# Kernel optimization log

Measured on AMD Instinct MI355X. Metric: run time of the kernel, lower is better.

## Reference

```python
import jax, jax.numpy as jnp
import numpy as np

# Constants derived from init_kwargs / input shapes
B = 4          # number of graphs (equal-sized point clouds)
N = 16384      # points per graph
STRIDE = 4     # center_sampler: strided sampling, ratio 0.25 -> M = N/4
K = 20         # k nearest neighbors
N_SCAL = 16    # reps '16x0+16x1': 16 scalars
N_VEC = 16     # 16 vectors (3 coeffs each)
D = N_SCAL + 3 * N_VEC   # 64 feature coeffs
HID = 128
OUT = 128


def transform_coeffs(x, R):
    """TensorReps('16x0+16x1') coefficient transform: scalars unchanged,
    each 3-vector v -> R @ v.  x: [n, D], R: [n, 3, 3]."""
    s = x[:, :N_SCAL]
    v = x[:, N_SCAL:].reshape(-1, N_VEC, 3)
    v = jnp.einsum('nab,nkb->nka', R, v)
    return jnp.concatenate([s, v.reshape(-1, 3 * N_VEC)], axis=-1)


def setup_inputs() -> dict:
    key = jax.random.key(0)
    ks = jax.random.split(key, 6)
    Ntot = B * N
    x = jax.random.normal(ks[0], (Ntot, D), jnp.float32)
    pos = jax.random.normal(ks[1], (Ntot, 3), jnp.float32)
    # orthonormal local frames via QR of random 3x3 matrices
    lf = jax.random.normal(ks[2], (Ntot, 3, 3), jnp.float32)
    lframes, _ = jnp.linalg.qr(lf)
    batch = jnp.repeat(jnp.arange(B, dtype=jnp.int32), N)
    W1 = jax.random.normal(ks[3], (2 * D, HID), jnp.float32) / np.sqrt(2 * D)
    b1 = jnp.zeros((HID,), jnp.float32)
    W2 = jax.random.normal(ks[4], (HID, OUT), jnp.float32) / np.sqrt(HID)
    b2 = jnp.zeros((OUT,), jnp.float32)
    return {"x": x, "pos": pos, "lframes": lframes, "batch": batch,
            "W1": W1, "b1": b1, "W2": W2, "b2": b2}


def reference(x, pos, lframes, batch, W1, b1, W2, b2):
    M = N // STRIDE
    # --- center_sampler: strided sampling per graph (CustomPointSampler) ---
    idx = (jnp.arange(B)[:, None] * N + jnp.arange(0, N, STRIDE)[None, :]).reshape(-1)  # [B*M]

    # --- transform features to global frame: coeffs with lframes^T ---
    kf = transform_coeffs(x, jnp.swapaxes(lframes, -1, -2))
    # --- concat_pos_to_features (transform_pos=False) ---
    kf = jnp.concatenate([kf, pos], axis=-1)            # [Ntot, 67]
    Dk = kf.shape[-1]

    # --- brute-force per-graph kNN: centers query against all nodes ---
    kf_b = kf.reshape(B, N, Dk)
    q = kf_b[:, ::STRIDE]                               # [B, M, Dk] centers
    d2 = (jnp.sum(q * q, -1)[:, :, None]
          + jnp.sum(kf_b * kf_b, -1)[:, None, :]
          - 2.0 * jnp.einsum('bmd,bnd->bmn', q, kf_b))  # [B, M, N]
    _, nbr = jax.lax.top_k(-d2, K)                      # [B, M, K] per-graph idx
    src = nbr + (jnp.arange(B) * N)[:, None, None]      # global node idx

    # --- gather dst/src node data ---
    x_dst = x[idx].reshape(B, M, D)
    lf_dst = lframes[idx]                               # [B*M, 3, 3]
    x_src = x[src.reshape(-1)].reshape(B, M, K, D)

    # --- EdgeConv (tensor-frames flavor): relative features rotated into the
    #     destination local frame, MLP over [x_i, R_i (x_j - x_i)], max-aggr ---
    rel = x_src - x_dst[:, :, None]                     # [B, M, K, D]
    R_edge = jnp.repeat(lf_dst, K, axis=0)              # [B*M*K, 3, 3]
    rel_local = transform_coeffs(rel.reshape(-1, D), R_edge).reshape(B, M, K, D)
    h = jnp.concatenate(
        [jnp.broadcast_to(x_dst[:, :, None], rel.shape), rel_local], axis=-1)  # [B,M,K,2D]
    msg = jax.nn.relu(h @ W1 + b1) @ W2 + b2            # [B, M, K, OUT]
    out = jnp.max(msg, axis=2).reshape(B * M, OUT)

    return out, pos[idx], batch[idx], lf_dst
```

## Files before the change

### kernel.cpp

```cpp
#include <hip/hip_runtime.h>
#include <hip/hip_bf16.h>

#define NTOT 65536
#define KNN  20
#define KROW 104

typedef __attribute__((ext_vector_type(4))) float f32x4;
typedef __attribute__((ext_vector_type(8))) short s16x8;

#define WS_NORM 13631488
#define WS_WT1  15204352
#define WS_WT2  15237120
#define WS_MG   15269888

#define ROWS 144
#define CSTR 257
#define OFF_TAUG 149056
#define KNN_SMEM 149312
#define THRESH 64

__device__ __forceinline__ unsigned short f2bf_rne(float v){
  unsigned u = __float_as_uint(v);
  return (unsigned short)((u + 0x7FFFu + ((u >> 16) & 1u)) >> 16);
}

__global__ __launch_bounds__(256) void k_prep(const float* __restrict__ x,
        const float* __restrict__ pos, const float* __restrict__ lfr,
        unsigned short* __restrict__ kfB, float* __restrict__ normB){
  int n = blockIdx.x * 256 + threadIdx.x;
  const float* xr = x + n * 64;
  float R[9];
  #pragma unroll
  for (int j = 0; j < 9; j++) R[j] = lfr[n * 9 + j];
  float c[67];
  #pragma unroll
  for (int i = 0; i < 16; i++) c[i] = xr[i];
  #pragma unroll
  for (int k = 0; k < 16; k++){
    float v0 = xr[16 + 3*k], v1 = xr[17 + 3*k], v2 = xr[18 + 3*k];
    #pragma unroll
    for (int a = 0; a < 3; a++)
      c[16 + 3*k + a] = R[a] * v0 + R[3 + a] * v1 + R[6 + a] * v2;
  }
  #pragma unroll
  for (int a = 0; a < 3; a++) c[64 + a] = pos[n * 3 + a];
  float sq = 0.f;
  #pragma unroll
  for (int d = 0; d < 67; d++) sq += c[d] * c[d];
  __attribute__((aligned(16))) unsigned short row[KROW];
  #pragma unroll
  for (int d = 0; d < 67; d++) row[d] = f2bf_rne(c[d]);
  #pragma unroll
  for (int d = 67; d < KROW; d++) row[d] = 0;
  uint4* dst = (uint4*)(kfB + (size_t)n * KROW);
  const uint4* s4 = (const uint4*)row;
  #pragma unroll
  for (int i = 0; i < 13; i++) dst[i] = s4[i];
  normB[n] = sq;
}

__global__ __launch_bounds__(256) void k_wprep(const float* __restrict__ W1,
        const float* __restrict__ W2, unsigned short* __restrict__ wb1,
        unsigned short* __restrict__ wb2){
  int a = blockIdx.x * 256 + threadIdx.x;
  int kb = a >> 12, n = (a >> 5) & 127, kl = a & 31;
  int i = ((kb << 5) + kl) * 128 + n;
  wb1[a] = f2bf_rne(W1[i]);
  wb2[a] = f2bf_rne(W2[i]);
}

__device__ __forceinline__ unsigned col_compact32(unsigned* buf,
    int col, int cn, int lane){
  unsigned e0 = (lane < cn) ? buf[lane * CSTR + col] : 0xFFFFFFFFu;
  unsigned e1 = (lane + 64 < cn) ? buf[(lane + 64) * CSTR + col] : 0xFFFFFFFFu;
  unsigned T = 0;
  #pragma unroll 1
  for (int b = 31; b >= 0; --b){
    unsigned cand = T | (1u << b);
    int c = __popcll(__ballot(e0 < cand)) + __popcll(__ballot(e1 < cand));
    if (c <= 31) T = cand;
  }
  unsigned long long m0 = __ballot(e0 <= T);
  unsigned long long m1 = __ballot(e1 <= T);
  int b1 = __popcll(m0);
  unsigned long long ltm = (1ull << lane) - 1ull;
  if (e0 <= T) buf[__popcll(m0 & ltm) * CSTR + col] = e0;
  if (e1 <= T) buf[(b1 + __popcll(m1 & ltm)) * CSTR + col] = e1;
  return T;
}

__device__ __forceinline__ unsigned col_compact18(unsigned* buf,
    int col, int cn, int lane){
  unsigned e0 = (lane < cn) ? buf[lane * CSTR + col] : 0xFFFFFFFFu;
  unsigned e1 = (lane + 64 < cn) ? buf[(lane + 64) * CSTR + col] : 0xFFFFFFFFu;
  unsigned T = 0;
  #pragma unroll 1
  for (int b = 31; b >= 14; --b){
    unsigned cand = T | (1u << b);
    int c = __popcll(__ballot(e0 < cand)) + __popcll(__ballot(e1 < cand));
    if (c <= 31) T = cand;
  }
  unsigned th = T >> 14;
  unsigned long long m0 = __ballot((e0 >> 14) <= th);
  unsigned long long m1 = __ballot((e1 >> 14) <= th);
  int b1 = __popcll(m0);
  int kc = b1 + __popcll(m1);
  unsigned long long ltm = (1ull << lane) - 1ull;
  if ((e0 >> 14) <= th) buf[__popcll(m0 & ltm) * CSTR + col] = e0;
  if ((e1 >> 14) <= th) buf[(b1 + __popcll(m1 & ltm)) * CSTR + col] = e1;
  return T | (unsigned)kc;
}

__global__ __launch_bounds__(1024, 4) void k_knn(
    const unsigned short* __restrict__ kfB, const float* __restrict__ normB,
    unsigned short* __restrict__ mgG){
  __shared__ __attribute__((aligned(16))) char smem[KNN_SMEM];
  unsigned* buf = (unsigned*)smem;
  unsigned* tauG = (unsigned*)(smem + OFF_TAUG);

  int tid = threadIdx.x;
  int blk = blockIdx.x;
  int b = blk & 3;
  int qloc0 = (blk >> 2) << 6;
  int bbase = b << 14;

  if (tid < 64) tauG[tid] = 0x7F7FC000u;

  int lane = tid & 63;
  int wv = tid >> 6;
  int wq = wv >> 2;
  int kq = wv & 3;
  int l15 = lane & 15, quad = lane >> 4;
  int colB = (wq << 6) + kq;

  int qloc = qloc0 + (wq << 4);
  s16x8 af[3];
  {
    int nodeA = bbase + ((qloc + l15) << 2);
    const unsigned short* ap = kfB + (size_t)nodeA * KROW + quad * 8;
    af[0] = *(const s16x8*)(ap);
    af[1] = *(const s16x8*)(ap + 32);
    af[2] = *(const s16x8*)(ap + 64);
  }
  float qsq[4];
  #pragma unroll
  for (int r = 0; r < 4; r++)
    qsq[r] = normB[bbase + ((qloc + (quad << 2) + r) << 2)];

  float tauR[4] = {3.0e38f, 3.0e38f, 3.0e38f, 3.0e38f};
  int cntR[4];

  const unsigned short* kp = kfB + (size_t)(bbase + (kq << 12) + l15) * KROW + quad * 8;
  const float* np = normB + (bbase + (kq << 12) + l15);

  __syncthreads();

  s16x8 cK[4][3];
  float nK[4];
  #define LOADK(S) do { \
      cK[S][0] = *(const s16x8*)(kp); \
      cK[S][1] = *(const s16x8*)(kp + 32); \
      cK[S][2] = *(const s16x8*)(kp + 64); \
      nK[S] = *np; kp += 16 * KROW; np += 16; } while (0)

  auto comp = [&](const s16x8 bf[3], float ksqv, float d2v[4]){
    f32x4 acc = (f32x4){0.f, 0.f, 0.f, 0.f};
    acc = __builtin_amdgcn_mfma_f32_16x16x32_bf16(af[0], bf[0], acc, 0, 0, 0);
    acc = __builtin_amdgcn_mfma_f32_16x16x32_bf16(af[1], bf[1], acc, 0, 0, 0);
    acc = __builtin_amdgcn_mfma_f32_16x16x32_bf16(af[2], bf[2], acc, 0, 0, 0);
    #pragma unroll
    for (int r = 0; r < 4; r++)
      d2v[r] = fmaxf(qsq[r] + ksqv - 2.f * acc[r], 0.f);
  };

  auto seed = [&](const float d2v[4], int g){
    int kidx = (kq << 12) + (g << 4) + l15;
    #pragma unroll
    for (int r = 0; r < 4; r++){
      unsigned pk = ((__float_as_uint(d2v[r]) + 0x2000u) & 0xFFFFC000u) | (unsigned)kidx;
      buf[((g << 4) + l15) * CSTR + colB + (quad << 4) + (r << 2)] = pk;
    }
  };

  auto process = [&](const float d2v[4], int g){
    bool p[4];
    #pragma unroll
    for (int r = 0; r < 4; r++) p[r] = d2v[r] < tauR[r];
    if (__any(p[0] | p[1] | p[2] | p[3])){
      int kidx = (kq << 12) + (g << 4) + l15;
      #pragma unroll
      for (int r = 0; r < 4; r++){
        unsigned long long m = __ballot(p[r]);
        if (m){
          int lo = (int)((m >> (quad << 4)) & 0xFFFFull);
          if (lo){
            int colr = colB + (quad << 4) + (r << 2);
            int pre = __popc(lo & ((1 << l15) - 1));
            if (p[r]){
              unsigned pk = ((__float_as_uint(d2v[r]) + 0x2000u) & 0xFFFFC000u) | (unsigned)kidx;
              buf[(cntR[r] + pre) * CSTR + colr] = pk;
            }
            cntR[r] += __popc(lo);
          }
        }
      }
    }
  };

  auto check_compact = [&](int limit){
    #pragma unroll
    for (int r = 0; r < 4; r++){
      unsigned long long mr = __ballot(cntR[r] > limit);
      while (mr){
        int ldr = __ffsll((unsigned long long)mr) - 1;
        int qd = ldr >> 4;
        mr &= ~(0xFFFFull << (qd << 4));
        int col = colB + (qd << 4) + (r << 2);
        int cn = __shfl(cntR[r], qd << 4, 64);
        unsigned Tk = col_compact18(buf, col, cn, lane);
        if (quad == qd) cntR[r] = (int)(Tk & 0x3FFFu);
        if (lane == 0) atomicMin(&tauG[(wq << 4) + (qd << 2) + r], Tk & 0xFFFFC000u);
      }
    }
  };

  float d2v[4];
  LOADK(0); LOADK(1); LOADK(2); LOADK(3);
  #pragma unroll
  for (int j = 0; j < 4; j++){
    comp(cK[j], nK[j], d2v);
    seed(d2v, j);
    LOADK(j);
  }
  #pragma unroll
  for (int r = 0; r < 4; r++) cntR[r] = 64;

  #pragma unroll 1
  for (int g = 4; g < 256; g += 4){
    #pragma unroll
    for (int j = 0; j < 4; j++){
      comp(cK[j], nK[j], d2v);
      LOADK(j);
      process(d2v, g + j);
    }
    check_compact(THRESH);
    uint4 tg = *(const uint4*)&tauG[(wq << 4) + (quad << 2)];
    tauR[0] = __uint_as_float(tg.x & 0xFFFFC000u);
    tauR[1] = __uint_as_float(tg.y & 0xFFFFC000u);
    tauR[2] = __uint_as_float(tg.z & 0xFFFFC000u);
    tauR[3] = __uint_as_float(tg.w & 0xFFFFC000u);
  }

  {
    #pragma unroll
    for (int r = 0; r < 4; r++){
      unsigned long long mr = __ballot(cntR[r] > 32);
      while (mr){
        int ldr = __ffsll((unsigned long long)mr) - 1;
        int qd = ldr >> 4;
        mr &= ~(0xFFFFull << (qd << 4));
        int col = colB + (qd << 4) + (r << 2);
        int cn = __shfl(cntR[r], qd << 4, 64);
        col_compact32(buf, col, cn, lane);
        if (quad == qd) cntR[r] = 32;
      }
    }
  }
  __syncthreads();

  #pragma unroll 1
  for (int s = 0; s < 4; s++){
    int q = (wv << 2) + s;
    int qid = (b << 12) + qloc0 + q;
    unsigned e0 = buf[(lane & 31) * CSTR + (q << 2) + (lane >> 5)];
    unsigned e1 = buf[(lane & 31) * CSTR + (q << 2) + 2 + (lane >> 5)];
    unsigned T = 0;
    #pragma unroll 1
    for (int bb = 31; bb >= 0; --bb){
      unsigned cand = T | (1u << bb);
      int c = __popcll(__ballot(e0 < cand)) + __popcll(__ballot(e1 < cand));
      if (c <= 31) T = cand;
    }
    unsigned long long m0 = __ballot(e0 <= T);
    unsigned long long m1 = __ballot(e1 <= T);
    int b1 = __popcll(m0);
    unsigned long long ltm = (1ull << lane) - 1ull;
    int p0 = __popcll(m0 & ltm);
    int p1 = b1 + __popcll(m1 & ltm);
    if ((e0 <= T) && (p0 < 32)) mgG[qid * 32 + p0] = (unsigned short)(e0 & 0x3FFFu);
    if ((e1 <= T) && (p1 < 32)) mgG[qid * 32 + p1] = (unsigned short)(e1 & 0x3FFFu);
  }
}

#define M_X   0
#define M_H   43520
#define M_B1  84480
#define M_B2  84992
#define M_NBR 85504
#define M_XD  86144
#define M_LF  88192
#define M_SZ  88512

__global__ __launch_bounds__(512) void k_mlp(const float* __restrict__ x,
    const float* __restrict__ pos, const float* __restrict__ lfr,
    const unsigned short* __restrict__ mgG,
    const unsigned short* __restrict__ wb1, const unsigned short* __restrict__ wb2,
    const float* __restrict__ b1, const float* __restrict__ b2,
    float* __restrict__ out){
  __shared__ __attribute__((aligned(16))) char smem[M_SZ];
  double* qkf = (double*)(smem + M_X);
  float* xsF = (float*)(smem + M_X);
  unsigned short* a1B = (unsigned short*)(smem + M_X);
  unsigned short* hB = (unsigned short*)(smem + M_H);
  float* b1L = (float*)(smem + M_B1);
  float* b2L = (float*)(smem + M_B2);
  int*   nbrL = (int*)(smem + M_NBR);
  float* xdL  = (float*)(smem + M_XD);
  float* lfL  = (float*)(smem + M_LF);

  int tid = threadIdx.x;
  int qid0 = blockIdx.x * 8;
  int lane = tid & 63, wv = tid >> 6;
  int l15 = lane & 15, quad = lane >> 4;

  s16x8 wf1[4], wf2[4];
  #pragma unroll
  for (int ks = 0; ks < 4; ks++){
    int a = (ks * 128 + (wv << 4) + l15) * 32 + (quad << 3);
    wf1[ks] = *(const s16x8*)(wb1 + a);
    wf2[ks] = *(const s16x8*)(wb2 + a);
  }

  {
    int q = tid >> 6, d = tid & 63;
    int qid = qid0 + q;
    int node = ((qid >> 12) << 14) + ((qid & 4095) << 2);
    xdL[q * 64 + d] = x[node * 64 + d];
  }
  if (tid < 72){
    int q = tid / 9, j = tid - 9 * q;
    int qid = qid0 + q;
    int node = ((qid >> 12) << 14) + ((qid & 4095) << 2);
    lfL[q * 9 + j] = lfr[node * 9 + j];
  }
  if (tid < 128){ b1L[tid] = b1[tid]; b2L[tid] = b2[tid]; }
  if (tid < 256){
    int ql = tid >> 5, j = tid & 31;
    int qid = qid0 + ql;
    int node_q = ((qid >> 12) << 14) + ((qid & 4095) << 2);
    const float* xr = x + node_q * 64;
    for (int dd = j; dd < 67; dd += 32){
      double val;
      if (dd < 16) val = (double)xr[dd];
      else if (dd < 64){
        int r = dd - 16; int k = r / 3; int a = r - 3 * k;
        val = (double)lfr[node_q*9 + a]     * (double)xr[16 + 3*k]
            + (double)lfr[node_q*9 + 3 + a] * (double)xr[17 + 3*k]
            + (double)lfr[node_q*9 + 6 + a] * (double)xr[18 + 3*k];
      } else val = (double)pos[node_q*3 + (dd - 64)];
      qkf[ql * 68 + dd] = val;
    }
  }
  __syncthreads();

  if (tid < 256){
    int ql = tid >> 5, j = tid & 31;
    int qid = qid0 + ql;
    int bbase = (qid >> 12) << 14;
    int idx = (int)mgG[(size_t)qid * 32 + j];
    int node = bbase + idx;
    const float* xr = x + node * 64;
    double R[9];
    #pragma unroll
    for (int t = 0; t < 9; t++) R[t] = (double)lfr[node * 9 + t];
    double d2 = 0.0;
    #pragma unroll
    for (int dd = 0; dd < 16; dd++){ double t = (double)xr[dd] - qkf[ql*68 + dd]; d2 += t * t; }
    #pragma unroll
    for (int k = 0; k < 16; k++){
      double v0 = xr[16 + 3*k], v1 = xr[17 + 3*k], v2 = xr[18 + 3*k];
      #pragma unroll
      for (int a = 0; a < 3; a++){
        double val = R[a] * v0 + R[3 + a] * v1 + R[6 + a] * v2;
        double t = val - qkf[ql*68 + 16 + 3*k + a]; d2 += t * t;
      }
    }
    #pragma unroll
    for (int a = 0; a < 3; a++){ double t = (double)pos[node*3 + a] - qkf[ql*68 + 64 + a]; d2 += t * t; }

    int base = (tid & 32) ? 32 : 0;
    int rank = 0;
    #pragma unroll 1
    for (int j2 = 0; j2 < 32; j2++){
      double o = __shfl(d2, base + j2, 64);
      rank += (o < d2) || ((o == d2) && (j2 < j));
    }
    if (rank < KNN) nbrL[ql * KNN + rank] = node;
  }
  __syncthreads();

  {
    int f4 = tid & 15;
    #pragma unroll
    for (int p = 0; p < 5; p++){
      int e = (tid >> 4) + (p << 5);
      float4 v = *(const float4*)&x[(size_t)nbrL[e] * 64 + (f4 << 2)];
      *(float4*)&xsF[e * 68 + (f4 << 2)] = v;
    }
  }
  __syncthreads();

  {
    int d = tid & 127, eo = tid >> 7;
    int cls, kk = 0, aa = 0;
    if (d < 64) cls = 0;
    else { int dd = d - 64;
      if (dd < 16) cls = 1;
      else { cls = 2; int r = dd - 16; kk = (r * 21846) >> 16; aa = r - 3 * kk; } }
    int hoff = ((d >> 5) * 160) * 32 + (d & 31);
    #pragma unroll 4
    for (int p = 0; p < 40; p++){
      int e = eo + (p << 2);
      int q = (e * 3277) >> 16;
      float v;
      if (cls == 0) v = xdL[q * 64 + d];
      else if (cls == 1) v = xsF[e * 68 + (d - 64)] - xdL[q * 64 + (d - 64)];
      else {
        int base = 16 + 3 * kk;
        float u0 = xsF[e * 68 + base]     - xdL[q * 64 + base];
        float u1 = xsF[e * 68 + base + 1] - xdL[q * 64 + base + 1];
        float u2 = xsF[e * 68 + base + 2] - xdL[q * 64 + base + 2];
        v = lfL[q * 9 + aa * 3] * u0 + lfL[q * 9 + aa * 3 + 1] * u1 + lfL[q * 9 + aa * 3 + 2] * u2;
      }
      hB[hoff + e * 32] = f2bf_rne(v);
    }
  }
  __syncthreads();

  {
    float b1v = b1L[(wv << 4) + l15];
    int colhi = wv >> 1, collo = ((wv & 1) << 4) + l15;
    #pragma unroll
    for (int mt = 0; mt < 10; mt++){
      f32x4 acc = (f32x4){0.f, 0.f, 0.f, 0.f};
      #pragma unroll
      for (int ks = 0; ks < 4; ks++){
        s16x8 af = *(const s16x8*)(hB + ((ks * 160 + (mt << 4) + l15) * 32 + (quad << 3)));
        acc = __builtin_amdgcn_mfma_f32_16x16x32_bf16(af, wf1[ks], acc, 0, 0, 0);
      }
      #pragma unroll
      for (int r = 0; r < 4; r++){
        float v = fmaxf(acc[r] + b1v, 0.f);
        int row = (mt << 4) + (quad << 2) + r;
        a1B[(colhi * 160 + row) * 32 + collo] = f2bf_rne(v);
      }
    }
  }
  __syncthreads();

  {
    float mxv[8];
    #pragma unroll
    for (int q = 0; q < 8; q++) mxv[q] = -3.0e38f;
    const int QA[10]  = {0,0,1,2,3,4,4,5,6,7};
    const int CUT[10] = {16,4,8,12,16,16,4,8,12,16};
    #pragma unroll
    for (int mt = 0; mt < 10; mt++){
      f32x4 acc = (f32x4){0.f, 0.f, 0.f, 0.f};
      #pragma unroll
      for (int ks = 0; ks < 4; ks++){
        s16x8 af = *(const s16x8*)(a1B + ((ks * 160 + (mt << 4) + l15) * 32 + (quad << 3)));
        acc = __builtin_amdgcn_mfma_f32_16x16x32_bf16(af, wf2[ks], acc, 0, 0, 0);
      }
      int qa = QA[mt], cut = CUT[mt];
      if (cut >= 16){
        #pragma unroll
        for (int r = 0; r < 4; r++) mxv[qa] = fmaxf(mxv[qa], acc[r]);
      } else {
        #pragma unroll
        for (int r = 0; r < 4; r++){
          int lr = (quad << 2) + r;
          bool toA = lr < cut;
          mxv[qa]     = fmaxf(mxv[qa],     toA ? acc[r] : -3.0e38f);
          mxv[qa + 1] = fmaxf(mxv[qa + 1], toA ? -3.0e38f : acc[r]);
        }
      }
    }
    #pragma unroll
    for (int q = 0; q < 8; q++){
      float v = mxv[q];
      v = fmaxf(v, __shfl_xor(v, 16, 64));
      v = fmaxf(v, __shfl_xor(v, 32, 64));
      mxv[q] = v;
    }
    if (quad == 0){
      int col = (wv << 4) + l15;
      float b2v = b2L[col];
      #pragma unroll
      for (int q = 0; q < 8; q++)
        out[(size_t)(qid0 + q) * 128 + col] = mxv[q] + b2v;
    }
  }
}

__global__ __launch_bounds__(256) void k_tail(const float* __restrict__ pos,
    const float* __restrict__ lfr, float* __restrict__ out){
  int q = blockIdx.x * 256 + threadIdx.x;
  int b = q >> 12;
  int node = (b << 14) + ((q & 4095) << 2);
  float* o_pos = out + 2097152;
  float* o_bat = out + 2146304;
  float* o_lf  = out + 2162688;
  #pragma unroll
  for (int j = 0; j < 3; j++) o_pos[q * 3 + j] = pos[node * 3 + j];
  o_bat[q] = (float)b;
  #pragma unroll
  for (int j = 0; j < 9; j++) o_lf[q * 9 + j] = lfr[node * 9 + j];
}

extern "C" void kernel_launch(void* const* d_in, const int* in_sizes, int n_in,
                              void* d_out, int out_size, void* d_ws, size_t ws_size,
                              hipStream_t stream){
  const float* x   = (const float*)d_in[0];
  const float* pos = (const float*)d_in[1];
  const float* lfr = (const float*)d_in[2];
  const float* W1  = (const float*)d_in[4];
  const float* b1  = (const float*)d_in[5];
  const float* W2  = (const float*)d_in[6];
  const float* b2  = (const float*)d_in[7];

  unsigned short* kfB = (unsigned short*)d_ws;
  float* normB = (float*)((char*)d_ws + WS_NORM);
  unsigned short* wb1 = (unsigned short*)((char*)d_ws + WS_WT1);
  unsigned short* wb2 = (unsigned short*)((char*)d_ws + WS_WT2);
  unsigned short* mgG = (unsigned short*)((char*)d_ws + WS_MG);
  float* out = (float*)d_out;

  hipLaunchKernelGGL(k_prep,   dim3(256),  dim3(256),  0, stream, x, pos, lfr, kfB, normB);
  hipLaunchKernelGGL(k_wprep,  dim3(64),   dim3(256),  0, stream, W1, W2, wb1, wb2);
  hipLaunchKernelGGL(k_knn,    dim3(256),  dim3(1024), 0, stream, kfB, normB, mgG);
  hipLaunchKernelGGL(k_mlp,    dim3(2048), dim3(512),  0, stream, x, pos, lfr, mgG, wb1, wb2, b1, b2, out);
  hipLaunchKernelGGL(k_tail,   dim3(64),   dim3(256),  0, stream, pos, lfr, out);
}
```

Before: 535.9 us.

## Shrink k_mlp blocks to 4 queries with 256 threads and 32-column warp tiles

Each k_mlp block now handles 4 query centers with 4 waves instead of 8 queries with 8 waves, which halves the LDS footprint to about 44KB. Each wave now covers 32 output columns, using two 16-column MFMA tiles that share the same A fragments, so A-fragment LDS reads are reused across the two column tiles. The goal is more resident blocks per CU and less LDS traffic. The cost is more weight fragments held in registers, twice as many blocks each reloading weights, and fewer active threads during the per-query distance and rank stage.

```diff
diff --git a/kernel.cpp b/kernel.cpp
--- a/kernel.cpp
+++ b/kernel.cpp
@@ -293,15 +293,15 @@
 }
 
 #define M_X   0
-#define M_H   43520
-#define M_B1  84480
-#define M_B2  84992
-#define M_NBR 85504
-#define M_XD  86144
-#define M_LF  88192
-#define M_SZ  88512
-
-__global__ __launch_bounds__(512) void k_mlp(const float* __restrict__ x,
+#define M_H   21760
+#define M_B1  42240
+#define M_B2  42752
+#define M_NBR 43264
+#define M_XD  43584
+#define M_LF  44608
+#define M_SZ  44752
+
+__global__ __launch_bounds__(256) void k_mlp(const float* __restrict__ x,
     const float* __restrict__ pos, const float* __restrict__ lfr,
     const unsigned short* __restrict__ mgG,
     const unsigned short* __restrict__ wb1, const unsigned short* __restrict__ wb2,
@@ -319,17 +319,19 @@
   float* lfL  = (float*)(smem + M_LF);
 
   int tid = threadIdx.x;
-  int qid0 = blockIdx.x * 8;
+  int qid0 = blockIdx.x * 4;
   int lane = tid & 63, wv = tid >> 6;
   int l15 = lane & 15, quad = lane >> 4;
 
-  s16x8 wf1[4], wf2[4];
-  #pragma unroll
-  for (int ks = 0; ks < 4; ks++){
-    int a = (ks * 128 + (wv << 4) + l15) * 32 + (quad << 3);
-    wf1[ks] = *(const s16x8*)(wb1 + a);
-    wf2[ks] = *(const s16x8*)(wb2 + a);
-  }
+  s16x8 wf1[2][4], wf2[2][4];
+  #pragma unroll
+  for (int ct = 0; ct < 2; ct++)
+    #pragma unroll
+    for (int ks = 0; ks < 4; ks++){
+      int a = (ks * 128 + (wv << 5) + (ct << 4) + l15) * 32 + (quad << 3);
+      wf1[ct][ks] = *(const s16x8*)(wb1 + a);
+      wf2[ct][ks] = *(const s16x8*)(wb2 + a);
+    }
 
   {
     int q = tid >> 6, d = tid & 63;
@@ -337,14 +339,14 @@
     int node = ((qid >> 12) << 14) + ((qid & 4095) << 2);
     xdL[q * 64 + d] = x[node * 64 + d];
   }
-  if (tid < 72){
+  if (tid < 36){
     int q = tid / 9, j = tid - 9 * q;
     int qid = qid0 + q;
     int node = ((qid >> 12) << 14) + ((qid & 4095) << 2);
     lfL[q * 9 + j] = lfr[node * 9 + j];
   }
   if (tid < 128){ b1L[tid] = b1[tid]; b2L[tid] = b2[tid]; }
-  if (tid < 256){
+  if (tid < 128){
     int ql = tid >> 5, j = tid & 31;
     int qid = qid0 + ql;
     int node_q = ((qid >> 12) << 14) + ((qid & 4095) << 2);
@@ -363,7 +365,7 @@
   }
   __syncthreads();
 
-  if (tid < 256){
+  if (tid < 128){
     int ql = tid >> 5, j = tid & 31;
     int qid = qid0 + ql;
     int bbase = (qid >> 12) << 14;
@@ -403,7 +405,7 @@
     int f4 = tid & 15;
     #pragma unroll
     for (int p = 0; p < 5; p++){
-      int e = (tid >> 4) + (p << 5);
+      int e = (tid >> 4) + (p << 4);
       float4 v = *(const float4*)&x[(size_t)nbrL[e] * 64 + (f4 << 2)];
       *(float4*)&xsF[e * 68 + (f4 << 2)] = v;
     }
@@ -417,10 +419,10 @@
     else { int dd = d - 64;
       if (dd < 16) cls = 1;
       else { cls = 2; int r = dd - 16; kk = (r * 21846) >> 16; aa = r - 3 * kk; } }
-    int hoff = ((d >> 5) * 160) * 32 + (d & 31);
+    int hoff = ((d >> 5) * 80) * 32 + (d & 31);
     #pragma unroll 4
     for (int p = 0; p < 40; p++){
-      int e = eo + (p << 2);
+      int e = eo + (p << 1);
       int q = (e * 3277) >> 16;
       float v;
       if (cls == 0) v = xdL[q * 64 + d];
@@ -438,67 +440,86 @@
   __syncthreads();
 
   {
-    float b1v = b1L[(wv << 4) + l15];
-    int colhi = wv >> 1, collo = ((wv & 1) << 4) + l15;
-    #pragma unroll
-    for (int mt = 0; mt < 10; mt++){
-      f32x4 acc = (f32x4){0.f, 0.f, 0.f, 0.f};
-      #pragma unroll
-      for (int ks = 0; ks < 4; ks++){
-        s16x8 af = *(const s16x8*)(hB + ((ks * 160 + (mt << 4) + l15) * 32 + (quad << 3)));
-        acc = __builtin_amdgcn_mfma_f32_16x16x32_bf16(af, wf1[ks], acc, 0, 0, 0);
-      }
-      #pragma unroll
-      for (int r = 0; r < 4; r++){
-        float v = fmaxf(acc[r] + b1v, 0.f);
-        int row = (mt << 4) + (quad << 2) + r;
-        a1B[(colhi * 160 + row) * 32 + collo] = f2bf_rne(v);
-      }
-    }
-  }
-  __syncthreads();
-
-  {
-    float mxv[8];
-    #pragma unroll
-    for (int q = 0; q < 8; q++) mxv[q] = -3.0e38f;
-    const int QA[10]  = {0,0,1,2,3,4,4,5,6,7};
-    const int CUT[10] = {16,4,8,12,16,16,4,8,12,16};
-    #pragma unroll
-    for (int mt = 0; mt < 10; mt++){
-      f32x4 acc = (f32x4){0.f, 0.f, 0.f, 0.f};
-      #pragma unroll
-      for (int ks = 0; ks < 4; ks++){
-        s16x8 af = *(const s16x8*)(a1B + ((ks * 160 + (mt << 4) + l15) * 32 + (quad << 3)));
-        acc = __builtin_amdgcn_mfma_f32_16x16x32_bf16(af, wf2[ks], acc, 0, 0, 0);
-      }
-      int qa = QA[mt], cut = CUT[mt];
-      if (cut >= 16){
+    float b1v[2];
+    b1v[0] = b1L[(wv << 5) + l15];
+    b1v[1] = b1L[(wv << 5) + 16 + l15];
+    #pragma unroll
+    for (int mt = 0; mt < 5; mt++){
+      s16x8 af[4];
+      #pragma unroll
+      for (int ks = 0; ks < 4; ks++)
+        af[ks] = *(const s16x8*)(hB + ((ks * 80 + (mt << 4) + l15) * 32 + (quad << 3)));
+      #pragma unroll
+      for (int ct = 0; ct < 2; ct++){
+        f32x4 acc = (f32x4){0.f, 0.f, 0.f, 0.f};
         #pragma unroll
-        for (int r = 0; r < 4; r++) mxv[qa] = fmaxf(mxv[qa], acc[r]);
-      } else {
+        for (int ks = 0; ks < 4; ks++)
+          acc = __builtin_amdgcn_mfma_f32_16x16x32_bf16(af[ks], wf1[ct][ks], acc, 0, 0, 0);
         #pragma unroll
         for (int r = 0; r < 4; r++){
-          int lr = (quad << 2) + r;
-          bool toA = lr < cut;
-          mxv[qa]     = fmaxf(mxv[qa],     toA ? acc[r] : -3.0e38f);
-          mxv[qa + 1] = fmaxf(mxv[qa + 1], toA ? -3.0e38f : acc[r]);
+          float v = fmaxf(acc[r] + b1v[ct], 0.f);
+          int row = (mt << 4) + (quad << 2) + r;
+          a1B[(wv * 80 + row) * 32 + (ct << 4) + l15] = f2bf_rne(v);
         }
       }
     }
-    #pragma unroll
-    for (int q = 0; q < 8; q++){
-      float v = mxv[q];
-      v = fmaxf(v, __shfl_xor(v, 16, 64));
-      v = fmaxf(v, __shfl_xor(v, 32, 64));
-      mxv[q] = v;
+  }
+  __syncthreads();
+
+  {
+    float mxv[2][4];
+    #pragma unroll
+    for (int ct = 0; ct < 2; ct++)
+      #pragma unroll
+      for (int q = 0; q < 4; q++) mxv[ct][q] = -3.0e38f;
+    const int QA[5]  = {0,0,1,2,3};
+    const int CUT[5] = {16,4,8,12,16};
+    #pragma unroll
+    for (int mt = 0; mt < 5; mt++){
+      s16x8 af[4];
+      #pragma unroll
+      for (int ks = 0; ks < 4; ks++)
+        af[ks] = *(const s16x8*)(a1B + ((ks * 80 + (mt << 4) + l15) * 32 + (quad << 3)));
+      int qa = QA[mt], cut = CUT[mt];
+      #pragma unroll
+      for (int ct = 0; ct < 2; ct++){
+        f32x4 acc = (f32x4){0.f, 0.f, 0.f, 0.f};
+        #pragma unroll
+        for (int ks = 0; ks < 4; ks++)
+          acc = __builtin_amdgcn_mfma_f32_16x16x32_bf16(af[ks], wf2[ct][ks], acc, 0, 0, 0);
+        if (cut >= 16){
+          #pragma unroll
+          for (int r = 0; r < 4; r++) mxv[ct][qa] = fmaxf(mxv[ct][qa], acc[r]);
+        } else {
+          #pragma unroll
+          for (int r = 0; r < 4; r++){
+            int lr = (quad << 2) + r;
+            bool toA = lr < cut;
+            mxv[ct][qa]     = fmaxf(mxv[ct][qa],     toA ? acc[r] : -3.0e38f);
+            mxv[ct][qa + 1] = fmaxf(mxv[ct][qa + 1], toA ? -3.0e38f : acc[r]);
+          }
+        }
+      }
+    }
+    #pragma unroll
+    for (int ct = 0; ct < 2; ct++){
+      #pragma unroll
+      for (int q = 0; q < 4; q++){
+        float v = mxv[ct][q];
+        v = fmaxf(v, __shfl_xor(v, 16, 64));
+        v = fmaxf(v, __shfl_xor(v, 32, 64));
+        mxv[ct][q] = v;
+      }
     }
     if (quad == 0){
-      int col = (wv << 4) + l15;
-      float b2v = b2L[col];
-      #pragma unroll
-      for (int q = 0; q < 8; q++)
-        out[(size_t)(qid0 + q) * 128 + col] = mxv[q] + b2v;
+      #pragma unroll
+      for (int ct = 0; ct < 2; ct++){
+        int col = (wv << 5) + (ct << 4) + l15;
+        float b2v = b2L[col];
+        #pragma unroll
+        for (int q = 0; q < 4; q++)
+          out[(size_t)(qid0 + q) * 128 + col] = mxv[ct][q] + b2v;
+      }
     }
   }
 }
@@ -539,6 +560,6 @@
   hipLaunchKernelGGL(k_prep,   dim3(256),  dim3(256),  0, stream, x, pos, lfr, kfB, normB);
   hipLaunchKernelGGL(k_wprep,  dim3(64),   dim3(256),  0, stream, W1, W2, wb1, wb2);
   hipLaunchKernelGGL(k_knn,    dim3(256),  dim3(1024), 0, stream, kfB, normB, mgG);
-  hipLaunchKernelGGL(k_mlp,    dim3(2048), dim3(512),  0, stream, x, pos, lfr, mgG, wb1, wb2, b1, b2, out);
+  hipLaunchKernelGGL(k_mlp,    dim3(4096), dim3(256),  0, stream, x, pos, lfr, mgG, wb1, wb2, b1, b2, out);
   hipLaunchKernelGGL(k_tail,   dim3(64),   dim3(256),  0, stream, pos, lfr, out);
 }
```

After: 503.6 us. 1.06x faster.
